# Kernel tuning notes

Hardware: AMD Instinct MI355X
Metric: run time of the kernel (lower is better)

## Reference

```python
import jax, jax.numpy as jnp
import numpy as np

B, T, I, H = 4096, 512, 4, 64  # batch, seq_len, input_size, hidden_size


def setup_inputs() -> dict:
    key = jax.random.key(0)
    ks = jax.random.split(key, 13)
    sc = 1.0 / np.sqrt(H)
    sc2 = 1.0 / np.sqrt(32)
    n = lambda k, shape, s: (jax.random.normal(k, shape, jnp.float32) * s)
    return {
        "x": jax.random.normal(ks[0], (B, T, I), jnp.float32),
        # PyTorch LSTM layout: gates stacked as [i, f, g, o] along first dim
        "w_ih0": n(ks[1], (4 * H, I), sc),
        "w_hh0": n(ks[2], (4 * H, H), sc),
        "b_ih0": n(ks[3], (4 * H,), sc),
        "b_hh0": n(ks[4], (4 * H,), sc),
        "w_ih1": n(ks[5], (4 * H, H), sc),
        "w_hh1": n(ks[6], (4 * H, H), sc),
        "b_ih1": n(ks[7], (4 * H,), sc),
        "b_hh1": n(ks[8], (4 * H,), sc),
        "fc1_w": n(ks[9], (32, H), sc),
        "fc1_b": n(ks[10], (32,), sc),
        "fc2_w": n(ks[11], (2, 32), sc2),
        "fc2_b": n(ks[12], (2,), sc2),
    }


def _lstm_layer(x, w_ih, w_hh, b_ih, b_hh):
    # x: [B, T, D_in] -> hidden sequence [B, T, H]
    Bq = x.shape[0]
    Hq = w_hh.shape[1]
    # Precompute input contribution for all timesteps in one GEMM
    pre = jnp.einsum('bti,gi->btg', x, w_ih) + b_ih + b_hh  # [B, T, 4H]
    pre = jnp.swapaxes(pre, 0, 1)  # [T, B, 4H] for scan

    def step(carry, xt):
        h, c = carry
        gates = xt + h @ w_hh.T  # [B, 4H]
        i, f, g, o = jnp.split(gates, 4, axis=-1)
        c_new = jax.nn.sigmoid(f) * c + jax.nn.sigmoid(i) * jnp.tanh(g)
        h_new = jax.nn.sigmoid(o) * jnp.tanh(c_new)
        return (h_new, c_new), h_new

    h0 = jnp.zeros((Bq, Hq), x.dtype)
    _, hs = jax.lax.scan(step, (h0, h0), pre)
    return jnp.swapaxes(hs, 0, 1)  # [B, T, H]


def reference(x, w_ih0, w_hh0, b_ih0, b_hh0, w_ih1, w_hh1, b_ih1, b_hh1,
              fc1_w, fc1_b, fc2_w, fc2_b):
    h1 = _lstm_layer(x, w_ih0, w_hh0, b_ih0, b_hh0)
    # dropout(p=0.2) between LSTM layers is inactive in eval mode
    h2 = _lstm_layer(h1, w_ih1, w_hh1, b_ih1, b_hh1)
    last = h2[:, -1, :]  # [B, H]
    y = jax.nn.relu(last @ fc1_w.T + fc1_b)
    return jax.nn.relu(y @ fc2_w.T + fc2_b)  # [B, 2]
```

## Files before the change

### kernel.cpp

```cpp
#include <hip/hip_runtime.h>

#define TT 512
#define MM 16

typedef _Float16 f16_t;
typedef f16_t f16x8 __attribute__((ext_vector_type(8)));
typedef float  f32x4 __attribute__((ext_vector_type(4)));

#define MFMA16(A, B, C) __builtin_amdgcn_mfma_f32_16x16x32_f16((A), (B), (C), 0, 0, 0)

__device__ __forceinline__ float fr(float x) { return __builtin_amdgcn_rcpf(x); }

__device__ __forceinline__ float cellEW(float pi, float pf, float pg, float po, float& c) {
    float A = __expf(-pf);
    float B = __expf(-pi);
    float C = __expf(2.f * pg);
    float ra = fr(1.f + A);
    float rb = fr((1.f + B) * (C + 1.f));
    float cn = fmaf(c, ra, (C - 1.f) * rb);
    c = cn;
    float D = __expf(-po);
    float E = __expf(2.f * cn);
    float rd = fr(1.f + D);
    float re = fr(E + 1.f);
    return rd * fmaf(-2.f, re, 1.f);
}

__device__ __forceinline__ f16x8 cvt8(const float* p) {
    f16x8 r;
#pragma unroll
    for (int e = 0; e < 8; ++e) r[e] = (f16_t)p[e];
    return r;
}

__device__ __forceinline__ f16x8 buildxf(float4 xq, int lq) {
    float v[4] = {xq.x, xq.y, xq.z, xq.w};
    f16x8 r;
#pragma unroll
    for (int e = 0; e < 8; ++e) r[e] = (e < 4 && lq == 0) ? (f16_t)v[e] : (f16_t)0.f;
    return r;
}


__global__ __launch_bounds__(512, 2) void lstm_f16(
    const float* __restrict__ x,
    const float* __restrict__ w_ih0, const float* __restrict__ w_hh0,
    const float* __restrict__ b_ih0, const float* __restrict__ b_hh0,
    const float* __restrict__ w_ih1, const float* __restrict__ w_hh1,
    const float* __restrict__ b_ih1, const float* __restrict__ b_hh1,
    const float* __restrict__ fc1_w, const float* __restrict__ fc1_b,
    const float* __restrict__ fc2_w, const float* __restrict__ fc2_b,
    float* __restrict__ out)
{
    __shared__ __align__(16) unsigned hpl[2][2][512];
    __shared__ __align__(16) float sH[MM * 68];
    __shared__ float sY[MM * 34];

    const int tid = threadIdx.x;
    const int l   = tid & 63;
    const int wv  = tid >> 6;
    const int rbase = blockIdx.x * MM;

    const int lc = l & 15;
    const int lq = l >> 4;
    const int chunk = l ^ lq;

    const bool isL1 = (wv >= 4);
    const int  ht   = wv & 3;
    const int  hidx = ht * 16 + lc;

    const int ktw = hidx >> 5;
    const int kk  = hidx & 31;
    const int ew  = kk & 7;
    const int kb  = kk >> 3;

    f16x8 wA[4][2], wB[4][2], wx[4];
    float bs[4];
#pragma unroll
    for (int g = 0; g < 4; ++g) {
        const int ga = g * 64 + hidx;
        if (isL1) {
#pragma unroll
            for (int kt = 0; kt < 2; ++kt)
                wA[g][kt] = cvt8(w_hh0 + ga * 64 + kt * 32 + lq * 8);
            float4 w4 = *(const float4*)(w_ih0 + ga * 4);
            wx[g] = buildxf(w4, lq);
            bs[g] = b_ih0[ga] + b_hh0[ga];
        } else {
#pragma unroll
            for (int kt = 0; kt < 2; ++kt) {
                wA[g][kt] = cvt8(w_ih1 + ga * 64 + kt * 32 + lq * 8);
                wB[g][kt] = cvt8(w_hh1 + ga * 64 + kt * 32 + lq * 8);
            }
            bs[g] = b_ih1[ga] + b_hh1[ga];
        }
    }

    for (int i = tid; i < 2 * 2 * 512; i += 512) ((unsigned*)hpl)[i] = 0;

    float c_st[4] = {0.f, 0.f, 0.f, 0.f};

    const float4* xg = (const float4*)x;
    const size_t xrow = (size_t)(rbase + lc) * TT;
    float4 xq0 = make_float4(0, 0, 0, 0), xq = make_float4(0, 0, 0, 0);
    if (isL1) { xq0 = xg[xrow + 0]; xq = xg[xrow + 1]; }

    __syncthreads();

    if (isL1) {
        f16x8 xf = buildxf(xq0, lq);
        f32x4 a[4];
#pragma unroll
        for (int g = 0; g < 4; ++g) {
#pragma unroll
            for (int q = 0; q < 4; ++q) a[g][q] = bs[g];
            a[g] = MFMA16(xf, wx[g], a[g]);
        }
        f16_t* dst = (f16_t*)hpl[0][0];
#pragma unroll
        for (int q = 0; q < 4; ++q) {
            float hv = cellEW(a[0][q], a[1][q], a[2][q], a[3][q], c_st[q]);
            const int lp = (lq * 4 + q) + 16 * kb;
            dst[ktw * 512 + (lp ^ kb) * 8 + ew] = (f16_t)hv;
        }
    }
    __syncthreads();

    int cur = 0;
    for (int t = 0; t < TT; ++t) {
        if (isL1) {
            if (t + 1 < TT) {
                const int tnext = (t + 2 < TT) ? t + 2 : TT - 1;
                float4 xq_new = xg[xrow + tnext];

                const f16_t* p1 = (const f16_t*)hpl[cur][0];
                f16x8 ah[2];
#pragma unroll
                for (int kt = 0; kt < 2; ++kt)
                    ah[kt] = *(const f16x8*)(p1 + kt * 512 + chunk * 8);
                f16x8 xf = buildxf(xq, lq);

                f32x4 a[4];
                __builtin_amdgcn_s_setprio(1);
#pragma unroll
                for (int g = 0; g < 4; ++g) {
#pragma unroll
                    for (int q = 0; q < 4; ++q) a[g][q] = bs[g];
                    a[g] = MFMA16(xf, wx[g], a[g]);
                    a[g] = MFMA16(ah[0], wA[g][0], a[g]);
                    a[g] = MFMA16(ah[1], wA[g][1], a[g]);
                }
                __builtin_amdgcn_s_setprio(0);

                f16_t* dst = (f16_t*)hpl[cur ^ 1][0];
#pragma unroll
                for (int q = 0; q < 4; ++q) {
                    float hv = cellEW(a[0][q], a[1][q], a[2][q], a[3][q], c_st[q]);
                    const int lp = (lq * 4 + q) + 16 * kb;
                    dst[ktw * 512 + (lp ^ kb) * 8 + ew] = (f16_t)hv;
                }
                xq = xq_new;
            }
        } else {
            const f16_t* p1 = (const f16_t*)hpl[cur][0];
            const f16_t* p2 = (const f16_t*)hpl[cur][1];
            f16x8 ah[2], ph[2];
#pragma unroll
            for (int kt = 0; kt < 2; ++kt) {
                ah[kt] = *(const f16x8*)(p1 + kt * 512 + chunk * 8);
                ph[kt] = *(const f16x8*)(p2 + kt * 512 + chunk * 8);
            }

            f32x4 a[4];
            __builtin_amdgcn_s_setprio(1);
#pragma unroll
            for (int g = 0; g < 4; ++g) {
#pragma unroll
                for (int q = 0; q < 4; ++q) a[g][q] = bs[g];
                a[g] = MFMA16(ah[0], wA[g][0], a[g]);
                a[g] = MFMA16(ah[1], wA[g][1], a[g]);
                a[g] = MFMA16(ph[0], wB[g][0], a[g]);
                a[g] = MFMA16(ph[1], wB[g][1], a[g]);
            }
            __builtin_amdgcn_s_setprio(0);

            f16_t* dst = (f16_t*)hpl[cur ^ 1][1];
#pragma unroll
            for (int q = 0; q < 4; ++q) {
                float hv = cellEW(a[0][q], a[1][q], a[2][q], a[3][q], c_st[q]);
                const int lp = (lq * 4 + q) + 16 * kb;
                dst[ktw * 512 + (lp ^ kb) * 8 + ew] = (f16_t)hv;
                if (t == TT - 1) sH[(lq * 4 + q) * 68 + hidx] = hv;
            }
        }
        cur ^= 1;
        __syncthreads();
    }

    {
        const int r = tid >> 5, mo = tid & 31;
        float s = fc1_b[mo];
#pragma unroll 8
        for (int k = 0; k < 64; ++k) s = fmaf(sH[r * 68 + k], fc1_w[mo * 64 + k], s);
        sY[r * 34 + mo] = fmaxf(s, 0.f);
    }
    __syncthreads();
    if (tid < 32) {
        const int r = tid >> 1, o = tid & 1;
        float s = fc2_b[o];
#pragma unroll 8
        for (int mo = 0; mo < 32; ++mo) s = fmaf(sY[r * 34 + mo], fc2_w[o * 32 + mo], s);
        out[(size_t)(rbase + r) * 2 + o] = fmaxf(s, 0.f);
    }
}

extern "C" void kernel_launch(void* const* d_in, const int* in_sizes, int n_in,
                              void* d_out, int out_size, void* d_ws, size_t ws_size,
                              hipStream_t stream) {
    const float* x     = (const float*)d_in[0];
    const float* w_ih0 = (const float*)d_in[1];
    const float* w_hh0 = (const float*)d_in[2];
    const float* b_ih0 = (const float*)d_in[3];
    const float* b_hh0 = (const float*)d_in[4];
    const float* w_ih1 = (const float*)d_in[5];
    const float* w_hh1 = (const float*)d_in[6];
    const float* b_ih1 = (const float*)d_in[7];
    const float* b_hh1 = (const float*)d_in[8];
    const float* fc1_w = (const float*)d_in[9];
    const float* fc1_b = (const float*)d_in[10];
    const float* fc2_w = (const float*)d_in[11];
    const float* fc2_b = (const float*)d_in[12];
    float* out = (float*)d_out;

    const int nB   = in_sizes[0] / (TT * 4);
    const int grid = nB / MM;

    lstm_f16<<<grid, 512, 0, stream>>>(x, w_ih0, w_hh0, b_ih0, b_hh0,
                                       w_ih1, w_hh1, b_ih1, b_hh1,
                                       fc1_w, fc1_b, fc2_w, fc2_b, out);
}
```

Measured before the change: 423.1 us.

## Halve batch rows per block and split elementwise work across lane halves

Measured after the change: 575.2 us. 35.9% more time.

```diff
diff --git a/kernel.cpp b/kernel.cpp
--- a/kernel.cpp
+++ b/kernel.cpp
@@ -1,7 +1,7 @@
 #include <hip/hip_runtime.h>
 
 #define TT 512
-#define MM 16
+#define MM 8
 
 typedef _Float16 f16_t;
 typedef f16_t f16x8 __attribute__((ext_vector_type(8)));
@@ -11,16 +11,25 @@
 
 __device__ __forceinline__ float fr(float x) { return __builtin_amdgcn_rcpf(x); }
 
-__device__ __forceinline__ float cellEW(float pi, float pf, float pg, float po, float& c) {
-    float A = __expf(-pf);
-    float B = __expf(-pi);
-    float C = __expf(2.f * pg);
+#if __has_builtin(__builtin_amdgcn_exp2f)
+__device__ __forceinline__ float ex2(float x) { return __builtin_amdgcn_exp2f(x); }
+#define EXS 1.44269504f
+#else
+__device__ __forceinline__ float ex2(float x) { return __expf(x); }
+#define EXS 1.0f
+#endif
+
+__device__ __forceinline__ float cellEW(float pi, float pf, float pg, float po,
+                                        float4 bsc, float& c) {
+    float A = ex2(fmaf(pf, -EXS, bsc.y));
+    float B = ex2(fmaf(pi, -EXS, bsc.x));
+    float C = ex2(fmaf(pg, 2.f * EXS, bsc.z));
     float ra = fr(1.f + A);
     float rb = fr((1.f + B) * (C + 1.f));
     float cn = fmaf(c, ra, (C - 1.f) * rb);
     c = cn;
-    float D = __expf(-po);
-    float E = __expf(2.f * cn);
+    float D = ex2(fmaf(po, -EXS, bsc.w));
+    float E = ex2(2.f * EXS * cn);
     float rd = fr(1.f + D);
     float re = fr(E + 1.f);
     return rd * fmaf(-2.f, re, 1.f);
@@ -33,16 +42,17 @@
     return r;
 }
 
-__device__ __forceinline__ f16x8 buildxf(float4 xq, int lq) {
+__device__ __forceinline__ f16x8 buildxf(float4 xq, int lq, int lc) {
     float v[4] = {xq.x, xq.y, xq.z, xq.w};
     f16x8 r;
 #pragma unroll
-    for (int e = 0; e < 8; ++e) r[e] = (e < 4 && lq == 0) ? (f16_t)v[e] : (f16_t)0.f;
+    for (int e = 0; e < 8; ++e)
+        r[e] = (e < 4 && lq == 0 && lc < 8) ? (f16_t)v[e] : (f16_t)0.f;
     return r;
 }
 
 
-__global__ __launch_bounds__(512, 2) void lstm_f16(
+__global__ __launch_bounds__(512, 4) void lstm_f16o(
     const float* __restrict__ x,
     const float* __restrict__ w_ih0, const float* __restrict__ w_hh0,
     const float* __restrict__ b_ih0, const float* __restrict__ b_hh0,
@@ -73,54 +83,82 @@
     const int kk  = hidx & 31;
     const int ew  = kk & 7;
     const int kb  = kk >> 3;
+    const int mb  = (lq & 1) * 4 + (l >> 5) * 2;
 
     f16x8 wA[4][2], wB[4][2], wx[4];
-    float bs[4];
-#pragma unroll
-    for (int g = 0; g < 4; ++g) {
-        const int ga = g * 64 + hidx;
-        if (isL1) {
-#pragma unroll
-            for (int kt = 0; kt < 2; ++kt)
-                wA[g][kt] = cvt8(w_hh0 + ga * 64 + kt * 32 + lq * 8);
+    float4 bsc;
+    {
+        float bi = 0, bf = 0, bg = 0, bo = 0;
+#pragma unroll
+        for (int g = 0; g < 4; ++g) {
+            const int ga = g * 64 + hidx;
+            float b;
+            if (isL1) {
+#pragma unroll
+                for (int kt = 0; kt < 2; ++kt)
+                    wA[g][kt] = cvt8(w_hh0 + ga * 64 + kt * 32 + lq * 8);
+                float4 w4 = *(const float4*)(w_ih0 + ga * 4);
+                wx[g] = buildxf(w4, lq, lc);
+                b = b_ih0[ga] + b_hh0[ga];
+            } else {
+#pragma unroll
+                for (int kt = 0; kt < 2; ++kt) {
+                    wA[g][kt] = cvt8(w_ih1 + ga * 64 + kt * 32 + lq * 8);
+                    wB[g][kt] = cvt8(w_hh1 + ga * 64 + kt * 32 + lq * 8);
+                }
+                b = b_ih1[ga] + b_hh1[ga];
+            }
+            if (g == 0) bi = b; else if (g == 1) bf = b; else if (g == 2) bg = b; else bo = b;
+        }
+        bsc = make_float4(-EXS * bi, -EXS * bf, 2.f * EXS * bg, -EXS * bo);
+    }
+    if (isL1) {
+#pragma unroll
+        for (int g = 0; g < 4; ++g) {
+            const int ga = g * 64 + hidx;
             float4 w4 = *(const float4*)(w_ih0 + ga * 4);
-            wx[g] = buildxf(w4, lq);
-            bs[g] = b_ih0[ga] + b_hh0[ga];
-        } else {
-#pragma unroll
-            for (int kt = 0; kt < 2; ++kt) {
-                wA[g][kt] = cvt8(w_ih1 + ga * 64 + kt * 32 + lq * 8);
-                wB[g][kt] = cvt8(w_hh1 + ga * 64 + kt * 32 + lq * 8);
-            }
-            bs[g] = b_ih1[ga] + b_hh1[ga];
+            float v[4] = {w4.x, w4.y, w4.z, w4.w};
+#pragma unroll
+            for (int e = 0; e < 8; ++e)
+                wx[g][e] = (e < 4 && lq == 0) ? (f16_t)v[e] : (f16_t)0.f;
         }
     }
 
     for (int i = tid; i < 2 * 2 * 512; i += 512) ((unsigned*)hpl)[i] = 0;
 
-    float c_st[4] = {0.f, 0.f, 0.f, 0.f};
+    float c_st[2] = {0.f, 0.f};
 
     const float4* xg = (const float4*)x;
-    const size_t xrow = (size_t)(rbase + lc) * TT;
+    const size_t xrow = (size_t)(rbase + (lc & 7)) * TT;
     float4 xq0 = make_float4(0, 0, 0, 0), xq = make_float4(0, 0, 0, 0);
     if (isL1) { xq0 = xg[xrow + 0]; xq = xg[xrow + 1]; }
 
     __syncthreads();
 
+    const int srcl = l & 31;
+
     if (isL1) {
-        f16x8 xf = buildxf(xq0, lq);
+        f16x8 xf = buildxf(xq0, lq, lc);
         f32x4 a[4];
 #pragma unroll
         for (int g = 0; g < 4; ++g) {
 #pragma unroll
-            for (int q = 0; q < 4; ++q) a[g][q] = bs[g];
+            for (int q = 0; q < 4; ++q) a[g][q] = 0.f;
             a[g] = MFMA16(xf, wx[g], a[g]);
         }
+        float pre[4][2];
+#pragma unroll
+        for (int g = 0; g < 4; ++g) {
+            float s2 = __shfl(a[g][2], srcl);
+            float s3 = __shfl(a[g][3], srcl);
+            pre[g][0] = (l < 32) ? a[g][0] : s2;
+            pre[g][1] = (l < 32) ? a[g][1] : s3;
+        }
         f16_t* dst = (f16_t*)hpl[0][0];
 #pragma unroll
-        for (int q = 0; q < 4; ++q) {
-            float hv = cellEW(a[0][q], a[1][q], a[2][q], a[3][q], c_st[q]);
-            const int lp = (lq * 4 + q) + 16 * kb;
+        for (int qq = 0; qq < 2; ++qq) {
+            float hv = cellEW(pre[0][qq], pre[1][qq], pre[2][qq], pre[3][qq], bsc, c_st[qq]);
+            const int lp = (mb + qq) + 16 * kb;
             dst[ktw * 512 + (lp ^ kb) * 8 + ew] = (f16_t)hv;
         }
     }
@@ -128,6 +166,7 @@
 
     int cur = 0;
     for (int t = 0; t < TT; ++t) {
+        f32x4 a[4];
         if (isL1) {
             if (t + 1 < TT) {
                 const int tnext = (t + 2 < TT) ? t + 2 : TT - 1;
@@ -138,25 +177,32 @@
 #pragma unroll
                 for (int kt = 0; kt < 2; ++kt)
                     ah[kt] = *(const f16x8*)(p1 + kt * 512 + chunk * 8);
-                f16x8 xf = buildxf(xq, lq);
-
-                f32x4 a[4];
+                f16x8 xf = buildxf(xq, lq, lc);
+
                 __builtin_amdgcn_s_setprio(1);
 #pragma unroll
                 for (int g = 0; g < 4; ++g) {
 #pragma unroll
-                    for (int q = 0; q < 4; ++q) a[g][q] = bs[g];
+                    for (int q = 0; q < 4; ++q) a[g][q] = 0.f;
                     a[g] = MFMA16(xf, wx[g], a[g]);
                     a[g] = MFMA16(ah[0], wA[g][0], a[g]);
                     a[g] = MFMA16(ah[1], wA[g][1], a[g]);
                 }
                 __builtin_amdgcn_s_setprio(0);
 
+                float pre[4][2];
+#pragma unroll
+                for (int g = 0; g < 4; ++g) {
+                    float s2 = __shfl(a[g][2], srcl);
+                    float s3 = __shfl(a[g][3], srcl);
+                    pre[g][0] = (l < 32) ? a[g][0] : s2;
+                    pre[g][1] = (l < 32) ? a[g][1] : s3;
+                }
                 f16_t* dst = (f16_t*)hpl[cur ^ 1][0];
 #pragma unroll
-                for (int q = 0; q < 4; ++q) {
-                    float hv = cellEW(a[0][q], a[1][q], a[2][q], a[3][q], c_st[q]);
-                    const int lp = (lq * 4 + q) + 16 * kb;
+                for (int qq = 0; qq < 2; ++qq) {
+                    float hv = cellEW(pre[0][qq], pre[1][qq], pre[2][qq], pre[3][qq], bsc, c_st[qq]);
+                    const int lp = (mb + qq) + 16 * kb;
                     dst[ktw * 512 + (lp ^ kb) * 8 + ew] = (f16_t)hv;
                 }
                 xq = xq_new;
@@ -170,13 +216,11 @@
                 ah[kt] = *(const f16x8*)(p1 + kt * 512 + chunk * 8);
                 ph[kt] = *(const f16x8*)(p2 + kt * 512 + chunk * 8);
             }
-
-            f32x4 a[4];
             __builtin_amdgcn_s_setprio(1);
 #pragma unroll
             for (int g = 0; g < 4; ++g) {
 #pragma unroll
-                for (int q = 0; q < 4; ++q) a[g][q] = bs[g];
+                for (int q = 0; q < 4; ++q) a[g][q] = 0.f;
                 a[g] = MFMA16(ah[0], wA[g][0], a[g]);
                 a[g] = MFMA16(ah[1], wA[g][1], a[g]);
                 a[g] = MFMA16(ph[0], wB[g][0], a[g]);
@@ -184,20 +228,29 @@
             }
             __builtin_amdgcn_s_setprio(0);
 
+            float pre[4][2];
+#pragma unroll
+            for (int g = 0; g < 4; ++g) {
+                float s2 = __shfl(a[g][2], srcl);
+                float s3 = __shfl(a[g][3], srcl);
+                pre[g][0] = (l < 32) ? a[g][0] : s2;
+                pre[g][1] = (l < 32) ? a[g][1] : s3;
+            }
             f16_t* dst = (f16_t*)hpl[cur ^ 1][1];
-#pragma unroll
-            for (int q = 0; q < 4; ++q) {
-                float hv = cellEW(a[0][q], a[1][q], a[2][q], a[3][q], c_st[q]);
-                const int lp = (lq * 4 + q) + 16 * kb;
+            const bool last = (t == TT - 1);
+#pragma unroll
+            for (int qq = 0; qq < 2; ++qq) {
+                float hv = cellEW(pre[0][qq], pre[1][qq], pre[2][qq], pre[3][qq], bsc, c_st[qq]);
+                const int lp = (mb + qq) + 16 * kb;
                 dst[ktw * 512 + (lp ^ kb) * 8 + ew] = (f16_t)hv;
-                if (t == TT - 1) sH[(lq * 4 + q) * 68 + hidx] = hv;
+                if (last) sH[(mb + qq) * 68 + hidx] = hv;
             }
         }
         cur ^= 1;
         __syncthreads();
     }
 
-    {
+    if (tid < MM * 32) {
         const int r = tid >> 5, mo = tid & 31;
         float s = fc1_b[mo];
 #pragma unroll 8
@@ -205,7 +258,7 @@
         sY[r * 34 + mo] = fmaxf(s, 0.f);
     }
     __syncthreads();
-    if (tid < 32) {
+    if (tid < MM * 2) {
         const int r = tid >> 1, o = tid & 1;
         float s = fc2_b[o];
 #pragma unroll 8
@@ -235,7 +288,7 @@
     const int nB   = in_sizes[0] / (TT * 4);
     const int grid = nB / MM;
 
-    lstm_f16<<<grid, 512, 0, stream>>>(x, w_ih0, w_hh0, b_ih0, b_hh0,
-                                       w_ih1, w_hh1, b_ih1, b_hh1,
-                                       fc1_w, fc1_b, fc2_w, fc2_b, out);
-}
+    lstm_f16o<<<grid, 512, 0, stream>>>(x, w_ih0, w_hh0, b_ih0, b_hh0,
+                                        w_ih1, w_hh1, b_ih1, b_hh1,
+                                        fc1_w, fc1_b, fc2_w, fc2_b, out);
+}
```

## Split LSTM timestep into two barrier phases, overlapping layer MFMA with elementwise

Applied to the files above, without the earlier changes.

New measurement: 451.9 us. +6.8%, slower.

```diff
diff --git a/kernel.cpp b/kernel.cpp
--- a/kernel.cpp
+++ b/kernel.cpp
@@ -11,16 +11,32 @@
 
 __device__ __forceinline__ float fr(float x) { return __builtin_amdgcn_rcpf(x); }
 
-__device__ __forceinline__ float cellEW(float pi, float pf, float pg, float po, float& c) {
-    float A = __expf(-pf);
-    float B = __expf(-pi);
-    float C = __expf(2.f * pg);
-    float ra = fr(1.f + A);
-    float rb = fr((1.f + B) * (C + 1.f));
-    float cn = fmaf(c, ra, (C - 1.f) * rb);
+#if __has_builtin(__builtin_amdgcn_exp2f)
+__device__ __forceinline__ float ex2(float x) { return __builtin_amdgcn_exp2f(x); }
+#define EXS 1.44269504f
+#else
+__device__ __forceinline__ float ex2(float x) { return __expf(x); }
+#define EXS 1.0f
+#endif
+
+__device__ __forceinline__ float cellEW(float pi, float pf, float pg, float po,
+                                        float4 bsc, float& c) {
+    float A = ex2(fmaf(pf, -EXS, bsc.y));
+    float B = ex2(fmaf(pi, -EXS, bsc.x));
+    float C = ex2(fmaf(pg, 2.f * EXS, bsc.z));
+    float u   = (1.f + B) * (C + 1.f);
+    float oa  = 1.f + A;
+    float num = fmaf(c * oa, u * fr(oa), oa * (C - 1.f));
+    float cn;
+    {
+        float nm = fmaf(c, u, oa * (C - 1.f));
+        float den = oa * u;
+        cn = nm * fr(den);
+    }
+    (void)num;
     c = cn;
-    float D = __expf(-po);
-    float E = __expf(2.f * cn);
+    float D = ex2(fmaf(po, -EXS, bsc.w));
+    float E = ex2(2.f * EXS * cn);
     float rd = fr(1.f + D);
     float re = fr(E + 1.f);
     return rd * fmaf(-2.f, re, 1.f);
@@ -42,7 +58,7 @@
 }
 
 
-__global__ __launch_bounds__(512, 2) void lstm_f16(
+__global__ __launch_bounds__(512, 2) void lstm_hs(
     const float* __restrict__ x,
     const float* __restrict__ w_ih0, const float* __restrict__ w_hh0,
     const float* __restrict__ b_ih0, const float* __restrict__ b_hh0,
@@ -52,7 +68,8 @@
     const float* __restrict__ fc2_w, const float* __restrict__ fc2_b,
     float* __restrict__ out)
 {
-    __shared__ __align__(16) unsigned hpl[2][2][512];
+    __shared__ __align__(16) unsigned hp1[2][512];
+    __shared__ __align__(16) unsigned hp2[512];
     __shared__ __align__(16) float sH[MM * 68];
     __shared__ float sY[MM * 34];
 
@@ -75,7 +92,7 @@
     const int kb  = kk >> 3;
 
     f16x8 wA[4][2], wB[4][2], wx[4];
-    float bs[4];
+    float bb[4];
 #pragma unroll
     for (int g = 0; g < 4; ++g) {
         const int ga = g * 64 + hidx;
@@ -85,24 +102,26 @@
                 wA[g][kt] = cvt8(w_hh0 + ga * 64 + kt * 32 + lq * 8);
             float4 w4 = *(const float4*)(w_ih0 + ga * 4);
             wx[g] = buildxf(w4, lq);
-            bs[g] = b_ih0[ga] + b_hh0[ga];
+            bb[g] = b_ih0[ga] + b_hh0[ga];
         } else {
 #pragma unroll
             for (int kt = 0; kt < 2; ++kt) {
                 wA[g][kt] = cvt8(w_ih1 + ga * 64 + kt * 32 + lq * 8);
                 wB[g][kt] = cvt8(w_hh1 + ga * 64 + kt * 32 + lq * 8);
             }
-            bs[g] = b_ih1[ga] + b_hh1[ga];
-        }
-    }
-
-    for (int i = tid; i < 2 * 2 * 512; i += 512) ((unsigned*)hpl)[i] = 0;
+            bb[g] = b_ih1[ga] + b_hh1[ga];
+        }
+    }
+    const float4 bsc = make_float4(-EXS * bb[0], -EXS * bb[1],
+                                   2.f * EXS * bb[2], -EXS * bb[3]);
+
+    hp2[tid] = 0;
 
     float c_st[4] = {0.f, 0.f, 0.f, 0.f};
 
     const float4* xg = (const float4*)x;
     const size_t xrow = (size_t)(rbase + lc) * TT;
-    float4 xq0 = make_float4(0, 0, 0, 0), xq = make_float4(0, 0, 0, 0);
+    float4 xq = make_float4(0, 0, 0, 0), xq0 = make_float4(0, 0, 0, 0);
     if (isL1) { xq0 = xg[xrow + 0]; xq = xg[xrow + 1]; }
 
     __syncthreads();
@@ -113,89 +132,103 @@
 #pragma unroll
         for (int g = 0; g < 4; ++g) {
 #pragma unroll
-            for (int q = 0; q < 4; ++q) a[g][q] = bs[g];
+            for (int q = 0; q < 4; ++q) a[g][q] = 0.f;
             a[g] = MFMA16(xf, wx[g], a[g]);
         }
-        f16_t* dst = (f16_t*)hpl[0][0];
+        f16_t* dst = (f16_t*)hp1[0];
 #pragma unroll
         for (int q = 0; q < 4; ++q) {
-            float hv = cellEW(a[0][q], a[1][q], a[2][q], a[3][q], c_st[q]);
+            float hv = cellEW(a[0][q], a[1][q], a[2][q], a[3][q], bsc, c_st[q]);
             const int lp = (lq * 4 + q) + 16 * kb;
             dst[ktw * 512 + (lp ^ kb) * 8 + ew] = (f16_t)hv;
         }
     }
     __syncthreads();
 
-    int cur = 0;
+    int p = 0;
+    f32x4 a2[4];
     for (int t = 0; t < TT; ++t) {
+        f32x4 a1[4];
         if (isL1) {
             if (t + 1 < TT) {
-                const int tnext = (t + 2 < TT) ? t + 2 : TT - 1;
-                float4 xq_new = xg[xrow + tnext];
-
-                const f16_t* p1 = (const f16_t*)hpl[cur][0];
+                const int tn = (t + 2 < TT) ? t + 2 : TT - 1;
+                float4 xn = xg[xrow + tn];
+
+                const f16_t* p1 = (const f16_t*)hp1[p];
                 f16x8 ah[2];
 #pragma unroll
                 for (int kt = 0; kt < 2; ++kt)
                     ah[kt] = *(const f16x8*)(p1 + kt * 512 + chunk * 8);
                 f16x8 xf = buildxf(xq, lq);
 
-                f32x4 a[4];
                 __builtin_amdgcn_s_setprio(1);
 #pragma unroll
                 for (int g = 0; g < 4; ++g) {
 #pragma unroll
-                    for (int q = 0; q < 4; ++q) a[g][q] = bs[g];
-                    a[g] = MFMA16(xf, wx[g], a[g]);
-                    a[g] = MFMA16(ah[0], wA[g][0], a[g]);
-                    a[g] = MFMA16(ah[1], wA[g][1], a[g]);
+                    for (int q = 0; q < 4; ++q) a1[g][q] = 0.f;
+                    a1[g] = MFMA16(xf, wx[g], a1[g]);
+                    a1[g] = MFMA16(ah[0], wA[g][0], a1[g]);
+                    a1[g] = MFMA16(ah[1], wA[g][1], a1[g]);
                 }
                 __builtin_amdgcn_s_setprio(0);
-
-                f16_t* dst = (f16_t*)hpl[cur ^ 1][0];
+                xq = xn;
+            }
+        } else {
+            if (t >= 1) {
+                f16_t* dst = (f16_t*)hp2;
 #pragma unroll
                 for (int q = 0; q < 4; ++q) {
-                    float hv = cellEW(a[0][q], a[1][q], a[2][q], a[3][q], c_st[q]);
+                    float hv = cellEW(a2[0][q], a2[1][q], a2[2][q], a2[3][q], bsc, c_st[q]);
                     const int lp = (lq * 4 + q) + 16 * kb;
                     dst[ktw * 512 + (lp ^ kb) * 8 + ew] = (f16_t)hv;
                 }
-                xq = xq_new;
+            }
+        }
+        __syncthreads();
+
+        if (isL1) {
+            if (t + 1 < TT) {
+                f16_t* dst = (f16_t*)hp1[p ^ 1];
+#pragma unroll
+                for (int q = 0; q < 4; ++q) {
+                    float hv = cellEW(a1[0][q], a1[1][q], a1[2][q], a1[3][q], bsc, c_st[q]);
+                    const int lp = (lq * 4 + q) + 16 * kb;
+                    dst[ktw * 512 + (lp ^ kb) * 8 + ew] = (f16_t)hv;
+                }
             }
         } else {
-            const f16_t* p1 = (const f16_t*)hpl[cur][0];
-            const f16_t* p2 = (const f16_t*)hpl[cur][1];
+            const f16_t* p1 = (const f16_t*)hp1[p];
+            const f16_t* p2 = (const f16_t*)hp2;
             f16x8 ah[2], ph[2];
 #pragma unroll
             for (int kt = 0; kt < 2; ++kt) {
                 ah[kt] = *(const f16x8*)(p1 + kt * 512 + chunk * 8);
                 ph[kt] = *(const f16x8*)(p2 + kt * 512 + chunk * 8);
             }
-
-            f32x4 a[4];
             __builtin_amdgcn_s_setprio(1);
 #pragma unroll
             for (int g = 0; g < 4; ++g) {
 #pragma unroll
-                for (int q = 0; q < 4; ++q) a[g][q] = bs[g];
-                a[g] = MFMA16(ah[0], wA[g][0], a[g]);
-                a[g] = MFMA16(ah[1], wA[g][1], a[g]);
-                a[g] = MFMA16(ph[0], wB[g][0], a[g]);
-                a[g] = MFMA16(ph[1], wB[g][1], a[g]);
+                for (int q = 0; q < 4; ++q) a2[g][q] = 0.f;
+                a2[g] = MFMA16(ah[0], wA[g][0], a2[g]);
+                a2[g] = MFMA16(ah[1], wA[g][1], a2[g]);
+                a2[g] = MFMA16(ph[0], wB[g][0], a2[g]);
+                a2[g] = MFMA16(ph[1], wB[g][1], a2[g]);
             }
             __builtin_amdgcn_s_setprio(0);
-
-            f16_t* dst = (f16_t*)hpl[cur ^ 1][1];
-#pragma unroll
-            for (int q = 0; q < 4; ++q) {
-                float hv = cellEW(a[0][q], a[1][q], a[2][q], a[3][q], c_st[q]);
-                const int lp = (lq * 4 + q) + 16 * kb;
-                dst[ktw * 512 + (lp ^ kb) * 8 + ew] = (f16_t)hv;
-                if (t == TT - 1) sH[(lq * 4 + q) * 68 + hidx] = hv;
-            }
-        }
-        cur ^= 1;
+        }
+        p ^= 1;
         __syncthreads();
     }
+
+    if (!isL1) {
+#pragma unroll
+        for (int q = 0; q < 4; ++q) {
+            float hv = cellEW(a2[0][q], a2[1][q], a2[2][q], a2[3][q], bsc, c_st[q]);
+            sH[(lq * 4 + q) * 68 + hidx] = hv;
+        }
+    }
+    __syncthreads();
 
     {
         const int r = tid >> 5, mo = tid & 31;
@@ -235,7 +268,7 @@
     const int nB   = in_sizes[0] / (TT * 4);
     const int grid = nB / MM;
 
-    lstm_f16<<<grid, 512, 0, stream>>>(x, w_ih0, w_hh0, b_ih0, b_hh0,
-                                       w_ih1, w_hh1, b_ih1, b_hh1,
-                                       fc1_w, fc1_b, fc2_w, fc2_b, out);
-}
+    lstm_hs<<<grid, 512, 0, stream>>>(x, w_ih0, w_hh0, b_ih0, b_hh0,
+                                      w_ih1, w_hh1, b_ih1, b_hh1,
+                                      fc1_w, fc1_b, fc2_w, fc2_b, out);
+}
```

## Swap MFMA operand roles, pack hidden state writes, and fold biases into exp2

Applied to the files above, without the earlier changes.

After: 404.1 us. 4.5% less time.

```diff
diff --git a/kernel.cpp b/kernel.cpp
--- a/kernel.cpp
+++ b/kernel.cpp
@@ -11,19 +11,39 @@
 
 __device__ __forceinline__ float fr(float x) { return __builtin_amdgcn_rcpf(x); }
 
-__device__ __forceinline__ float cellEW(float pi, float pf, float pg, float po, float& c) {
-    float A = __expf(-pf);
-    float B = __expf(-pi);
-    float C = __expf(2.f * pg);
-    float ra = fr(1.f + A);
-    float rb = fr((1.f + B) * (C + 1.f));
-    float cn = fmaf(c, ra, (C - 1.f) * rb);
+#if __has_builtin(__builtin_amdgcn_exp2f)
+__device__ __forceinline__ float ex2(float x) { return __builtin_amdgcn_exp2f(x); }
+#define EXS 1.44269504f
+#else
+__device__ __forceinline__ float ex2(float x) { return __expf(x); }
+#define EXS 1.0f
+#endif
+
+#if __has_builtin(__builtin_amdgcn_cvt_pkrtz)
+__device__ __forceinline__ unsigned pk2(float a, float b) {
+    auto p = __builtin_amdgcn_cvt_pkrtz(a, b);
+    return __builtin_bit_cast(unsigned, p);
+}
+#else
+__device__ __forceinline__ unsigned pk2(float a, float b) {
+    unsigned short ha = __builtin_bit_cast(unsigned short, (f16_t)a);
+    unsigned short hb = __builtin_bit_cast(unsigned short, (f16_t)b);
+    return (unsigned)ha | ((unsigned)hb << 16);
+}
+#endif
+
+__device__ __forceinline__ float cellEW(float pi, float pf, float pg, float po,
+                                        float4 bq, float& c) {
+    float A = ex2(fmaf(pf, -EXS, bq.y));
+    float B = ex2(fmaf(pi, -EXS, bq.x));
+    float C = ex2(fmaf(pg, 2.f * EXS, bq.z));
+    float oa = 1.f + A;
+    float u  = (1.f + B) * (C + 1.f);
+    float cn = fmaf(c, u, oa * (C - 1.f)) * fr(oa * u);
     c = cn;
-    float D = __expf(-po);
-    float E = __expf(2.f * cn);
-    float rd = fr(1.f + D);
-    float re = fr(E + 1.f);
-    return rd * fmaf(-2.f, re, 1.f);
+    float D = ex2(fmaf(po, -EXS, bq.w));
+    float E = ex2(fminf(2.f * EXS * cn, 30.f));
+    return (E - 1.f) * fr((1.f + D) * (E + 1.f));
 }
 
 __device__ __forceinline__ f16x8 cvt8(const float* p) {
@@ -42,7 +62,7 @@
 }
 
 
-__global__ __launch_bounds__(512, 2) void lstm_f16(
+__global__ __launch_bounds__(512, 2) void lstm_swp(
     const float* __restrict__ x,
     const float* __restrict__ w_ih0, const float* __restrict__ w_hh0,
     const float* __restrict__ b_ih0, const float* __restrict__ b_hh0,
@@ -52,7 +72,8 @@
     const float* __restrict__ fc2_w, const float* __restrict__ fc2_b,
     float* __restrict__ out)
 {
-    __shared__ __align__(16) unsigned hpl[2][2][512];
+    __shared__ __align__(16) unsigned h1p[2][512];
+    __shared__ __align__(16) unsigned h2p[2][512];
     __shared__ __align__(16) float sH[MM * 68];
     __shared__ float sY[MM * 34];
 
@@ -63,137 +84,131 @@
 
     const int lc = l & 15;
     const int lq = l >> 4;
-    const int chunk = l ^ lq;
-
     const bool isL1 = (wv >= 4);
-    const int  ht   = wv & 3;
-    const int  hidx = ht * 16 + lc;
-
-    const int ktw = hidx >> 5;
-    const int kk  = hidx & 31;
-    const int ew  = kk & 7;
-    const int kb  = kk >> 3;
-
-    f16x8 wA[4][2], wB[4][2], wx[4];
-    float bs[4];
+    const int wsub = wv & 3;
+    const int hc0  = wsub * 16 + lq * 4;
+    const int swz  = (lc & 7) << 4;
+
+    const int rdo0 = (lc * 128 + 0 * 64 + lq * 16) ^ swz;
+    const int rdo1 = (lc * 128 + 1 * 64 + lq * 16) ^ swz;
+    const int wro  = (lc * 128 + hc0 * 2) ^ swz;
+
+    f16x8 wA[4][2];
+    f16x8 wB[4][2];
+    f16x8 wx[4];
+    float4 bq[4];
 #pragma unroll
     for (int g = 0; g < 4; ++g) {
-        const int ga = g * 64 + hidx;
+        const int grow = (g * 64 + wsub * 16 + lc) * 64 + lq * 8;
         if (isL1) {
-#pragma unroll
-            for (int kt = 0; kt < 2; ++kt)
-                wA[g][kt] = cvt8(w_hh0 + ga * 64 + kt * 32 + lq * 8);
-            float4 w4 = *(const float4*)(w_ih0 + ga * 4);
-            wx[g] = buildxf(w4, lq);
-            bs[g] = b_ih0[ga] + b_hh0[ga];
+            wA[g][0] = cvt8(w_hh0 + grow);
+            wA[g][1] = cvt8(w_hh0 + grow + 32);
+            const int ga = (g * 64 + wsub * 16 + lc) * 4;
+#pragma unroll
+            for (int e = 0; e < 8; ++e)
+                wx[g][e] = (e < 4 && lq == 0) ? (f16_t)w_ih0[ga + e] : (f16_t)0.f;
         } else {
-#pragma unroll
-            for (int kt = 0; kt < 2; ++kt) {
-                wA[g][kt] = cvt8(w_ih1 + ga * 64 + kt * 32 + lq * 8);
-                wB[g][kt] = cvt8(w_hh1 + ga * 64 + kt * 32 + lq * 8);
-            }
-            bs[g] = b_ih1[ga] + b_hh1[ga];
+            wA[g][0] = cvt8(w_ih1 + grow);
+            wA[g][1] = cvt8(w_ih1 + grow + 32);
+            wB[g][0] = cvt8(w_hh1 + grow);
+            wB[g][1] = cvt8(w_hh1 + grow + 32);
         }
     }
-
-    for (int i = tid; i < 2 * 2 * 512; i += 512) ((unsigned*)hpl)[i] = 0;
+#pragma unroll
+    for (int q = 0; q < 4; ++q) {
+        const int hc = hc0 + q;
+        float b[4];
+#pragma unroll
+        for (int g = 0; g < 4; ++g) {
+            const int ga = g * 64 + hc;
+            b[g] = isL1 ? (b_ih0[ga] + b_hh0[ga]) : (b_ih1[ga] + b_hh1[ga]);
+        }
+        bq[q] = make_float4(-EXS * b[0], -EXS * b[1], 2.f * EXS * b[2], -EXS * b[3]);
+    }
 
     float c_st[4] = {0.f, 0.f, 0.f, 0.f};
+    const f32x4 z4 = {0.f, 0.f, 0.f, 0.f};
 
     const float4* xg = (const float4*)x;
     const size_t xrow = (size_t)(rbase + lc) * TT;
     float4 xq0 = make_float4(0, 0, 0, 0), xq = make_float4(0, 0, 0, 0);
     if (isL1) { xq0 = xg[xrow + 0]; xq = xg[xrow + 1]; }
 
-    __syncthreads();
-
     if (isL1) {
         f16x8 xf = buildxf(xq0, lq);
         f32x4 a[4];
 #pragma unroll
-        for (int g = 0; g < 4; ++g) {
-#pragma unroll
-            for (int q = 0; q < 4; ++q) a[g][q] = bs[g];
-            a[g] = MFMA16(xf, wx[g], a[g]);
-        }
-        f16_t* dst = (f16_t*)hpl[0][0];
-#pragma unroll
-        for (int q = 0; q < 4; ++q) {
-            float hv = cellEW(a[0][q], a[1][q], a[2][q], a[3][q], c_st[q]);
-            const int lp = (lq * 4 + q) + 16 * kb;
-            dst[ktw * 512 + (lp ^ kb) * 8 + ew] = (f16_t)hv;
-        }
+        for (int g = 0; g < 4; ++g) a[g] = MFMA16(wx[g], xf, z4);
+        float hv[4];
+#pragma unroll
+        for (int q = 0; q < 4; ++q)
+            hv[q] = cellEW(a[0][q], a[1][q], a[2][q], a[3][q], bq[q], c_st[q]);
+        uint2 w2 = make_uint2(pk2(hv[0], hv[1]), pk2(hv[2], hv[3]));
+        *(uint2*)((char*)h1p[0] + wro) = w2;
+    } else {
+        h2p[0][tid] = 0;
+        h2p[0][256 + tid] = 0;
     }
     __syncthreads();
 
-    int cur = 0;
+    int p = 0;
     for (int t = 0; t < TT; ++t) {
         if (isL1) {
             if (t + 1 < TT) {
-                const int tnext = (t + 2 < TT) ? t + 2 : TT - 1;
-                float4 xq_new = xg[xrow + tnext];
-
-                const f16_t* p1 = (const f16_t*)hpl[cur][0];
-                f16x8 ah[2];
-#pragma unroll
-                for (int kt = 0; kt < 2; ++kt)
-                    ah[kt] = *(const f16x8*)(p1 + kt * 512 + chunk * 8);
+                const char* pl = (const char*)h1p[p];
+                f16x8 hf0 = *(const f16x8*)(pl + rdo0);
+                f16x8 hf1 = *(const f16x8*)(pl + rdo1);
+                const int tn = (t + 2 < TT) ? t + 2 : TT - 1;
+                float4 xn = xg[xrow + tn];
                 f16x8 xf = buildxf(xq, lq);
 
                 f32x4 a[4];
                 __builtin_amdgcn_s_setprio(1);
 #pragma unroll
                 for (int g = 0; g < 4; ++g) {
-#pragma unroll
-                    for (int q = 0; q < 4; ++q) a[g][q] = bs[g];
-                    a[g] = MFMA16(xf, wx[g], a[g]);
-                    a[g] = MFMA16(ah[0], wA[g][0], a[g]);
-                    a[g] = MFMA16(ah[1], wA[g][1], a[g]);
+                    a[g] = MFMA16(wx[g], xf, z4);
+                    a[g] = MFMA16(wA[g][0], hf0, a[g]);
+                    a[g] = MFMA16(wA[g][1], hf1, a[g]);
                 }
                 __builtin_amdgcn_s_setprio(0);
 
-                f16_t* dst = (f16_t*)hpl[cur ^ 1][0];
-#pragma unroll
-                for (int q = 0; q < 4; ++q) {
-                    float hv = cellEW(a[0][q], a[1][q], a[2][q], a[3][q], c_st[q]);
-                    const int lp = (lq * 4 + q) + 16 * kb;
-                    dst[ktw * 512 + (lp ^ kb) * 8 + ew] = (f16_t)hv;
-                }
-                xq = xq_new;
+                float hv[4];
+#pragma unroll
+                for (int q = 0; q < 4; ++q)
+                    hv[q] = cellEW(a[0][q], a[1][q], a[2][q], a[3][q], bq[q], c_st[q]);
+                uint2 w2 = make_uint2(pk2(hv[0], hv[1]), pk2(hv[2], hv[3]));
+                *(uint2*)((char*)h1p[p ^ 1] + wro) = w2;
+                xq = xn;
             }
         } else {
-            const f16_t* p1 = (const f16_t*)hpl[cur][0];
-            const f16_t* p2 = (const f16_t*)hpl[cur][1];
-            f16x8 ah[2], ph[2];
-#pragma unroll
-            for (int kt = 0; kt < 2; ++kt) {
-                ah[kt] = *(const f16x8*)(p1 + kt * 512 + chunk * 8);
-                ph[kt] = *(const f16x8*)(p2 + kt * 512 + chunk * 8);
-            }
+            const char* pl1 = (const char*)h1p[p];
+            const char* pl2 = (const char*)h2p[p];
+            f16x8 hf0 = *(const f16x8*)(pl1 + rdo0);
+            f16x8 hf1 = *(const f16x8*)(pl1 + rdo1);
+            f16x8 gf0 = *(const f16x8*)(pl2 + rdo0);
+            f16x8 gf1 = *(const f16x8*)(pl2 + rdo1);
 
             f32x4 a[4];
             __builtin_amdgcn_s_setprio(1);
 #pragma unroll
             for (int g = 0; g < 4; ++g) {
-#pragma unroll
-                for (int q = 0; q < 4; ++q) a[g][q] = bs[g];
-                a[g] = MFMA16(ah[0], wA[g][0], a[g]);
-                a[g] = MFMA16(ah[1], wA[g][1], a[g]);
-                a[g] = MFMA16(ph[0], wB[g][0], a[g]);
-                a[g] = MFMA16(ph[1], wB[g][1], a[g]);
+                a[g] = MFMA16(wA[g][0], hf0, z4);
+                a[g] = MFMA16(wA[g][1], hf1, a[g]);
+                a[g] = MFMA16(wB[g][0], gf0, a[g]);
+                a[g] = MFMA16(wB[g][1], gf1, a[g]);
             }
             __builtin_amdgcn_s_setprio(0);
 
-            f16_t* dst = (f16_t*)hpl[cur ^ 1][1];
-#pragma unroll
-            for (int q = 0; q < 4; ++q) {
-                float hv = cellEW(a[0][q], a[1][q], a[2][q], a[3][q], c_st[q]);
-                const int lp = (lq * 4 + q) + 16 * kb;
-                dst[ktw * 512 + (lp ^ kb) * 8 + ew] = (f16_t)hv;
-                if (t == TT - 1) sH[(lq * 4 + q) * 68 + hidx] = hv;
-            }
+            float hv[4];
+#pragma unroll
+            for (int q = 0; q < 4; ++q)
+                hv[q] = cellEW(a[0][q], a[1][q], a[2][q], a[3][q], bq[q], c_st[q]);
+            uint2 w2 = make_uint2(pk2(hv[0], hv[1]), pk2(hv[2], hv[3]));
+            *(uint2*)((char*)h2p[p ^ 1] + wro) = w2;
+            if (t == TT - 1)
+                *(float4*)&sH[lc * 68 + hc0] = make_float4(hv[0], hv[1], hv[2], hv[3]);
         }
-        cur ^= 1;
+        p ^= 1;
         __syncthreads();
     }
 
@@ -235,7 +250,7 @@
     const int nB   = in_sizes[0] / (TT * 4);
     const int grid = nB / MM;
 
-    lstm_f16<<<grid, 512, 0, stream>>>(x, w_ih0, w_hh0, b_ih0, b_hh0,
+    lstm_swp<<<grid, 512, 0, stream>>>(x, w_ih0, w_hh0, b_ih0, b_hh0,
                                        w_ih1, w_hh1, b_ih1, b_hh1,
                                        fc1_w, fc1_b, fc2_w, fc2_b, out);
 }
```
